# Optimization experiments

Hardware: AMD Instinct MI355X
Metric: run time of the kernel (lower is better)

The kernel has to match this reference:

```python
import jax, jax.numpy as jnp
import numpy as np

N, E, F, H = 50000, 800000, 128, 128


def setup_inputs() -> dict:
    key = jax.random.key(0)
    ks = jax.random.split(key, 12)
    senders = jax.random.randint(ks[2], (E,), 0, N)
    receivers = jnp.sort(jax.random.randint(ks[3], (E,), 0, N))
    # ensure segment ids span full node range so segment_sum covers all N rows
    receivers = receivers.at[0].set(0).at[-1].set(N - 1)
    s = 0.05
    return {
        "nodes": jax.random.normal(ks[0], (N, F), jnp.float32),
        "edges": jax.random.normal(ks[1], (E, F), jnp.float32),
        "senders": senders,
        "receivers": receivers,
        "Wm1": jax.random.normal(ks[4], (3 * F, H), jnp.float32) * s,
        "bm1": jnp.zeros((H,), jnp.float32),
        "Wm2": jax.random.normal(ks[5], (H, H), jnp.float32) * s,
        "bm2": jnp.zeros((H,), jnp.float32),
        "Wu1": jax.random.normal(ks[6], (F + H, H), jnp.float32) * s,
        "bu1": jnp.zeros((H,), jnp.float32),
        "Wu2": jax.random.normal(ks[7], (H, H), jnp.float32) * s,
        "bu2": jnp.zeros((H,), jnp.float32),
    }


def reference(nodes, edges, senders, receivers, Wm1, bm1, Wm2, bm2, Wu1, bu1, Wu2, bu2):
    n = nodes.shape[0]
    sender_feat = nodes[senders]      # [E, F] gather
    receiver_feat = nodes[receivers]  # [E, F] gather
    msg_in = jnp.concatenate([sender_feat, receiver_feat, edges], axis=-1)  # [E, 3F]
    messages = jax.nn.swish(msg_in @ Wm1 + bm1) @ Wm2 + bm2                 # [E, H]
    aggregated = jax.ops.segment_sum(messages, receivers, num_segments=n)   # [N, H]
    upd_in = jnp.concatenate([nodes, aggregated], axis=-1)                   # [N, F+H]
    return jax.nn.swish(upd_in @ Wu1 + bu1) @ Wu2 + bu2                      # [N, H]
```

## Files before the change

kernel.cpp:

```cpp
#include <hip/hip_runtime.h>
#include <hip/hip_bf16.h>


typedef __bf16 bf16_t;
typedef __bf16 bf16x8 __attribute__((ext_vector_type(8)));
typedef __bf16 bf16x4 __attribute__((ext_vector_type(4)));
typedef float f32x4 __attribute__((ext_vector_type(4)));

#define MFMA16(a, b, c) __builtin_amdgcn_mfma_f32_16x16x32_bf16((a), (b), (c), 0, 0, 0)

__device__ __forceinline__ bf16x8 cvt_bf16x8(f32x4 lo, f32x4 hi) {
  bf16x8 r;
  r[0] = (bf16_t)lo[0]; r[1] = (bf16_t)lo[1]; r[2] = (bf16_t)lo[2]; r[3] = (bf16_t)lo[3];
  r[4] = (bf16_t)hi[0]; r[5] = (bf16_t)hi[1]; r[6] = (bf16_t)hi[2]; r[7] = (bf16_t)hi[3];
  return r;
}

__device__ __forceinline__ float swishf(float x) { return x / (1.0f + __expf(-x)); }

__device__ __forceinline__ int pst_idx(int col, int e) {
  const int unit = (e >> 3) ^ (col & 7) ^ ((col >> 3) & 7);
  return col * 64 + unit * 8 + (e & 7);
}

__global__ void prep_kernel(const float* __restrict__ Wm1, const float* __restrict__ Wm2,
                            const float* __restrict__ Wu1, const float* __restrict__ Wu2,
                            const float* __restrict__ bm2,
                            bf16_t* __restrict__ WmabT, bf16_t* __restrict__ Wm1cT,
                            bf16_t* __restrict__ Wu1aT, bf16_t* __restrict__ WcT,
                            bf16_t* __restrict__ Wu2T, float* __restrict__ bvec) {
  const int t0 = blockIdx.x * blockDim.x + threadIdx.x;
  const int stride = gridDim.x * blockDim.x;
  for (int i = t0; i < 256 * 128; i += stride) {
    const int n = i >> 7, k = i & 127;
    const float v = (n < 128) ? Wm1[k * 128 + n] : Wm1[(128 + k) * 128 + (n - 128)];
    WmabT[i] = (bf16_t)v;
  }
  for (int i = t0; i < 128 * 128; i += stride) {
    const int n = i >> 7, k = i & 127;
    Wm1cT[i] = (bf16_t)Wm1[(256 + k) * 128 + n];
    Wu1aT[i] = (bf16_t)Wu1[k * 128 + n];
    Wu2T[i]  = (bf16_t)Wu2[k * 128 + n];
  }
  for (int i = t0; i < 128 * 128; i += stride) {
    const int r = i >> 7, c = i & 127;
    float acc = 0.f;
    for (int k = 0; k < 128; ++k) acc += Wm2[r * 128 + k] * Wu1[(128 + k) * 128 + c];
    WcT[c * 128 + r] = (bf16_t)acc;
  }
  if (t0 < 128) {
    float acc = 0.f;
    for (int k = 0; k < 128; ++k) acc += bm2[k] * Wu1[(128 + k) * 128 + t0];
    bvec[t0] = acc;
  }
}

__global__ __launch_bounds__(256) void node_pre_kernel(const float* __restrict__ nodes,
                                                       const bf16_t* __restrict__ WmabT,
                                                       const float* __restrict__ bm1,
                                                       bf16_t* __restrict__ P, const int nN) {
  const int tid = threadIdx.x;
  const int l = tid & 63, w = tid >> 6;
  const int wr = w >> 1, wc = w & 1;
  const int lr = l & 15, lk = l >> 4;
  const int half = blockIdx.y;
  const int r0 = blockIdx.x * 128 + wr * 64;
  const bf16_t* WT = WmabT + half * (128 * 128);

  f32x4 acc[4][4] = {};
#pragma unroll
  for (int ks = 0; ks < 4; ++ks) {
    bf16x8 a[4], b[4];
#pragma unroll
    for (int m = 0; m < 4; ++m) {
      int r = r0 + m * 16 + lr;
      if (r >= nN) r = nN - 1;
      const float* p = nodes + (long)r * 128 + ks * 32 + lk * 8;
      a[m] = cvt_bf16x8(*(const f32x4*)p, *(const f32x4*)(p + 4));
    }
#pragma unroll
    for (int n = 0; n < 4; ++n)
      b[n] = *(const bf16x8*)(WT + (wc * 64 + n * 16 + lr) * 128 + ks * 32 + lk * 8);
#pragma unroll
    for (int m = 0; m < 4; ++m)
#pragma unroll
      for (int n = 0; n < 4; ++n)
        acc[m][n] = MFMA16(a[m], b[n], acc[m][n]);
  }
#pragma unroll
  for (int m = 0; m < 4; ++m)
#pragma unroll
    for (int n = 0; n < 4; ++n)
#pragma unroll
      for (int j = 0; j < 4; ++j) {
        const int r = r0 + m * 16 + lk * 4 + j;
        const int c = wc * 64 + n * 16 + lr;
        const float bias = (half == 0) ? bm1[c] : 0.f;
        if (r < nN) P[(long)r * 256 + half * 128 + c] = (bf16_t)(acc[m][n][j] + bias);
      }
}

__global__ __launch_bounds__(256, 3) void edge_kernel(
    const float* __restrict__ edges, const int* __restrict__ senders,
    const int* __restrict__ receivers, const bf16_t* __restrict__ P,
    const bf16_t* __restrict__ Wm1cT, float* __restrict__ S, float* __restrict__ deg,
    const int ntiles) {
  __shared__ bf16_t Ws[128 * 128];
  __shared__ bf16_t PsT[128 * 64];
  __shared__ int runidL[64];
  __shared__ int runstartL[65];
  __shared__ int nrunsL;
  const int tid = threadIdx.x;
  const int lane = tid & 63, w = tid >> 6;
  const int lr = lane & 15, lk = lane >> 4;

#pragma unroll
  for (int i = 0; i < 8; ++i) {
    const int g = tid + i * 256;
    const int r = g >> 4, c = g & 15;
    const bf16x8 v = *(const bf16x8*)(Wm1cT + r * 128 + c * 8);
    *(bf16x8*)&Ws[r * 128 + ((c ^ (r & 15)) * 8)] = v;
  }

  const int nb = gridDim.x;
  const int cb = (blockIdx.x & 7) * (nb >> 3) + (blockIdx.x >> 3);
  const int q = ntiles / nb, r2 = ntiles % nb;
  const int tstart = cb * q + (cb < r2 ? cb : r2);
  const int tcnt = q + (cb < r2 ? 1 : 0);

  __syncthreads();

  for (int ti = 0; ti < tcnt; ++ti) {
    const long e0 = (long)(tstart + ti) * 64;
    const int eg = w * 16 + lr;

    const int sn = senders[e0 + eg];
    const int rn = receivers[e0 + eg];

    f32x4 Bf[4][2];
#pragma unroll
    for (int kc = 0; kc < 4; ++kc) {
      const f32x4* p = (const f32x4*)(edges + (e0 + eg) * 128 + kc * 32 + lk * 8);
      Bf[kc][0] = __builtin_nontemporal_load(p);
      Bf[kc][1] = __builtin_nontemporal_load(p + 1);
    }
    bf16x4 pa[8], pb[8];
#pragma unroll
    for (int m = 0; m < 8; ++m) {
      pa[m] = *(const bf16x4*)(P + (long)sn * 256 + m * 16 + lk * 4);
      pb[m] = *(const bf16x4*)(P + (long)rn * 256 + 128 + m * 16 + lk * 4);
    }

    if (w == 0) {
      const int myrcv = receivers[e0 + lane];
      const int prev = (lane == 0) ? -1 : receivers[e0 + lane - 1];
      const int head = (myrcv != prev) ? 1 : 0;
      const unsigned long long mask = __ballot(head);
      const int nruns = __popcll(mask);
      if (lane == 0) { nrunsL = nruns; runstartL[nruns] = 64; }
      if (head) {
        const int pre = __popcll(mask & ((1ull << lane) - 1));
        runidL[pre] = myrcv;
        runstartL[pre] = lane;
      }
    }

    f32x4 acc[8] = {};
#pragma unroll
    for (int kc = 0; kc < 4; ++kc) {
      const bf16x8 bb = cvt_bf16x8(Bf[kc][0], Bf[kc][1]);
#pragma unroll
      for (int m = 0; m < 8; ++m) {
        const bf16x8 aW = *(const bf16x8*)&Ws[(m * 16 + lr) * 128 + (((kc * 4 + lk) ^ lr) * 8)];
        acc[m] = MFMA16(aW, bb, acc[m]);
      }
    }

#pragma unroll
    for (int m = 0; m < 8; ++m)
#pragma unroll
      for (int j = 0; j < 4; ++j) {
        const int outcol = m * 16 + lk * 4 + j;
        const float x = acc[m][j] + (float)pa[m][j] + (float)pb[m][j];
        PsT[pst_idx(outcol, eg)] = (bf16_t)swishf(x);
      }
    __syncthreads();

    const int nruns = nrunsL;
    for (int nt = 0; nt * 16 < nruns; ++nt) {
      const int myrun = nt * 16 + lr;
      int lo = 64, hi = 64, myid = -1;
      if (myrun < nruns) {
        lo = runstartL[myrun];
        hi = runstartL[myrun + 1];
        myid = runidL[myrun];
      }
      f32x4 accS[2] = {};
#pragma unroll
      for (int kc = 0; kc < 2; ++kc) {
        bf16x8 bR;
#pragma unroll
        for (int j = 0; j < 8; ++j) {
          const int e = kc * 32 + lk * 8 + j;
          bR[j] = (e >= lo && e < hi) ? (bf16_t)1.0f : (bf16_t)0.0f;
        }
#pragma unroll
        for (int t = 0; t < 2; ++t) {
          const int col = (2 * w + t) * 16 + lr;
          const int unit = (kc * 4 + lk) ^ (col & 7) ^ ((col >> 3) & 7);
          const bf16x8 aH = *(const bf16x8*)&PsT[col * 64 + unit * 8];
          accS[t] = MFMA16(aH, bR, accS[t]);
        }
      }
      if (myrun < nruns) {
        const long base = (long)myid * 128;
        const bool boundary = (myrun == 0) || (myrun == nruns - 1);
#pragma unroll
        for (int t = 0; t < 2; ++t) {
          const int col0 = (2 * w + t) * 16 + lk * 4;
          if (boundary) {
#pragma unroll
            for (int j = 0; j < 4; ++j) unsafeAtomicAdd(&S[base + col0 + j], accS[t][j]);
          } else {
            *(f32x4*)(S + base + col0) = accS[t];
          }
        }
      }
    }

    if (tid < nruns) {
      const float len = (float)(runstartL[tid + 1] - runstartL[tid]);
      const int node = runidL[tid];
      if (tid == 0 || tid == nruns - 1) unsafeAtomicAdd(&deg[node], len);
      else deg[node] = len;
    }
    __syncthreads();
  }
}

__global__ __launch_bounds__(256) void node_out_kernel(
    const float* __restrict__ nodes, const float* __restrict__ S,
    const float* __restrict__ deg, const float* __restrict__ bvec,
    const float* __restrict__ bu1, const float* __restrict__ bu2,
    const bf16_t* __restrict__ Wu1aT, const bf16_t* __restrict__ WcT,
    const bf16_t* __restrict__ Wu2T, float* __restrict__ out, const int nN) {
  __shared__ bf16_t Hs[128 * 128];
  const int tid = threadIdx.x;
  const int l = tid & 63, w = tid >> 6;
  const int wr = w >> 1, wc = w & 1;
  const int lr = l & 15, lk = l >> 4;
  const int r0 = blockIdx.x * 128;

  f32x4 acc[4][4] = {};
#pragma unroll
  for (int src = 0; src < 2; ++src) {
    const float* X = src ? S : nodes;
    const bf16_t* WT = src ? WcT : Wu1aT;
#pragma unroll
    for (int ks = 0; ks < 4; ++ks) {
      bf16x8 a[4], b[4];
#pragma unroll
      for (int m = 0; m < 4; ++m) {
        int r = r0 + wr * 64 + m * 16 + lr;
        if (r >= nN) r = nN - 1;
        const float* p = X + (long)r * 128 + ks * 32 + lk * 8;
        a[m] = cvt_bf16x8(*(const f32x4*)p, *(const f32x4*)(p + 4));
      }
#pragma unroll
      for (int n = 0; n < 4; ++n)
        b[n] = *(const bf16x8*)(WT + (wc * 64 + n * 16 + lr) * 128 + ks * 32 + lk * 8);
#pragma unroll
      for (int m = 0; m < 4; ++m)
#pragma unroll
        for (int n = 0; n < 4; ++n)
          acc[m][n] = MFMA16(a[m], b[n], acc[m][n]);
    }
  }

#pragma unroll
  for (int m = 0; m < 4; ++m)
#pragma unroll
    for (int n = 0; n < 4; ++n)
#pragma unroll
      for (int j = 0; j < 4; ++j) {
        const int row = wr * 64 + m * 16 + lk * 4 + j;
        const int gr = r0 + row;
        const int col = wc * 64 + n * 16 + lr;
        const float dg = (gr < nN) ? deg[gr] : 0.f;
        const float x = acc[m][n][j] + bu1[col] + dg * bvec[col];
        Hs[row * 128 + (col ^ ((row & 7) << 3))] = (bf16_t)swishf(x);
      }
  __syncthreads();

  f32x4 acc2[4][4] = {};
#pragma unroll
  for (int ks = 0; ks < 4; ++ks) {
    bf16x8 a[4], b[4];
#pragma unroll
    for (int m = 0; m < 4; ++m) {
      const int r = wr * 64 + m * 16 + lr;
      a[m] = *(const bf16x8*)&Hs[r * 128 + ((ks * 32 + lk * 8) ^ ((r & 7) << 3))];
    }
#pragma unroll
    for (int n = 0; n < 4; ++n)
      b[n] = *(const bf16x8*)(Wu2T + (wc * 64 + n * 16 + lr) * 128 + ks * 32 + lk * 8);
#pragma unroll
    for (int m = 0; m < 4; ++m)
#pragma unroll
      for (int n = 0; n < 4; ++n)
        acc2[m][n] = MFMA16(a[m], b[n], acc2[m][n]);
  }

#pragma unroll
  for (int m = 0; m < 4; ++m)
#pragma unroll
    for (int n = 0; n < 4; ++n)
#pragma unroll
      for (int j = 0; j < 4; ++j) {
        const int row = r0 + wr * 64 + m * 16 + lk * 4 + j;
        const int col = wc * 64 + n * 16 + lr;
        if (row < nN) out[(long)row * 128 + col] = acc2[m][n][j] + bu2[col];
      }
}

extern "C" void kernel_launch(void* const* d_in, const int* in_sizes, int n_in,
                              void* d_out, int out_size, void* d_ws, size_t ws_size,
                              hipStream_t stream) {
  const float* nodes = (const float*)d_in[0];
  const float* edges = (const float*)d_in[1];
  const int* senders = (const int*)d_in[2];
  const int* receivers = (const int*)d_in[3];
  const float* Wm1 = (const float*)d_in[4];
  const float* bm1 = (const float*)d_in[5];
  const float* Wm2 = (const float*)d_in[6];
  const float* bm2 = (const float*)d_in[7];
  const float* Wu1 = (const float*)d_in[8];
  const float* bu1 = (const float*)d_in[9];
  const float* Wu2 = (const float*)d_in[10];
  const float* bu2 = (const float*)d_in[11];
  const int nN = in_sizes[0] / 128;
  const int nE = in_sizes[1] / 128;

  char* ws = (char*)d_ws;
  bf16_t* P = (bf16_t*)ws;
  float* S = (float*)(ws + (size_t)nN * 256 * 2);
  float* deg = S + (size_t)nN * 128;
  bf16_t* WmabT = (bf16_t*)(deg + nN);
  bf16_t* Wm1cT = WmabT + 256 * 128;
  bf16_t* Wu1aT = Wm1cT + 128 * 128;
  bf16_t* WcT = Wu1aT + 128 * 128;
  bf16_t* Wu2T = WcT + 128 * 128;
  float* bvec = (float*)(Wu2T + 128 * 128);

  hipMemsetAsync(S, 0, (size_t)nN * 129 * 4, stream);
  hipLaunchKernelGGL(prep_kernel, dim3(128), dim3(256), 0, stream,
                     Wm1, Wm2, Wu1, Wu2, bm2, WmabT, Wm1cT, Wu1aT, WcT, Wu2T, bvec);
  hipLaunchKernelGGL(node_pre_kernel, dim3((nN + 127) / 128, 2), dim3(256), 0, stream,
                     nodes, WmabT, bm1, P, nN);
  hipLaunchKernelGGL(edge_kernel, dim3(768), dim3(256), 0, stream,
                     edges, senders, receivers, P, Wm1cT, S, deg, nE / 64);
  hipLaunchKernelGGL(node_out_kernel, dim3((nN + 127) / 128), dim3(256), 0, stream,
                     nodes, S, deg, bvec, bu1, bu2, Wu1aT, WcT, Wu2T, (float*)d_out, nN);
}
```

Before: 287.1 us.

## Prefetch next edge tile's indices and features; replace memset with zero kernel

The edge kernel now loads the next tile's sender/receiver indices and edge feature rows into registers while the current tile is being processed, software-pipelining global memory latency across iterations. The hipMemsetAsync for the accumulator buffer is replaced with a custom vectorized zero kernel, possibly to avoid memset API overhead. The prefetch raises register pressure (an extra 8 f32x4 per lane), which could lower occupancy.

New measurement: 424.5 us. +47.8%, slower.

```diff
diff --git a/kernel.cpp b/kernel.cpp
--- a/kernel.cpp
+++ b/kernel.cpp
@@ -21,6 +21,12 @@
 __device__ __forceinline__ int pst_idx(int col, int e) {
   const int unit = (e >> 3) ^ (col & 7) ^ ((col >> 3) & 7);
   return col * 64 + unit * 8 + (e & 7);
+}
+
+__global__ __launch_bounds__(256) void zero_kernel(float* __restrict__ p, const long nvec) {
+  const long t0 = (long)blockIdx.x * blockDim.x + threadIdx.x;
+  const long stride = (long)gridDim.x * blockDim.x;
+  for (long i = t0; i < nvec; i += stride) *(f32x4*)(p + i * 4) = f32x4{0.f, 0.f, 0.f, 0.f};
 }
 
 __global__ void prep_kernel(const float* __restrict__ Wm1, const float* __restrict__ Wm2,
@@ -130,25 +136,42 @@
 
   __syncthreads();
 
-  for (int ti = 0; ti < tcnt; ++ti) {
-    const long e0 = (long)(tstart + ti) * 64;
-    const int eg = w * 16 + lr;
-
-    const int sn = senders[e0 + eg];
-    const int rn = receivers[e0 + eg];
-
-    f32x4 Bf[4][2];
+  const int eg = w * 16 + lr;
+
+  long e0 = (long)tstart * 64;
+  int sn = 0, rn = 0;
+  f32x4 Bf[4][2] = {};
+  if (tcnt > 0) {
+    sn = senders[e0 + eg];
+    rn = receivers[e0 + eg];
 #pragma unroll
     for (int kc = 0; kc < 4; ++kc) {
       const f32x4* p = (const f32x4*)(edges + (e0 + eg) * 128 + kc * 32 + lk * 8);
       Bf[kc][0] = __builtin_nontemporal_load(p);
       Bf[kc][1] = __builtin_nontemporal_load(p + 1);
     }
+  }
+
+  for (int ti = 0; ti < tcnt; ++ti) {
     bf16x4 pa[8], pb[8];
 #pragma unroll
     for (int m = 0; m < 8; ++m) {
       pa[m] = *(const bf16x4*)(P + (long)sn * 256 + m * 16 + lk * 4);
       pb[m] = *(const bf16x4*)(P + (long)rn * 256 + 128 + m * 16 + lk * 4);
+    }
+
+    const long e0n = e0 + 64;
+    int sn_n = 0, rn_n = 0;
+    f32x4 Bfn[4][2] = {};
+    if (ti + 1 < tcnt) {
+      sn_n = senders[e0n + eg];
+      rn_n = receivers[e0n + eg];
+#pragma unroll
+      for (int kc = 0; kc < 4; ++kc) {
+        const f32x4* p = (const f32x4*)(edges + (e0n + eg) * 128 + kc * 32 + lk * 8);
+        Bfn[kc][0] = __builtin_nontemporal_load(p);
+        Bfn[kc][1] = __builtin_nontemporal_load(p + 1);
+      }
     }
 
     if (w == 0) {
@@ -235,6 +258,13 @@
       else deg[node] = len;
     }
     __syncthreads();
+
+    e0 = e0n; sn = sn_n; rn = rn_n;
+#pragma unroll
+    for (int kc = 0; kc < 4; ++kc) {
+      Bf[kc][0] = Bfn[kc][0];
+      Bf[kc][1] = Bfn[kc][1];
+    }
   }
 }
 
@@ -352,7 +382,8 @@
   bf16_t* Wu2T = WcT + 128 * 128;
   float* bvec = (float*)(Wu2T + 128 * 128);
 
-  hipMemsetAsync(S, 0, (size_t)nN * 129 * 4, stream);
+  hipLaunchKernelGGL(zero_kernel, dim3(1024), dim3(256), 0, stream,
+                     S, (long)nN * 129 / 4);
   hipLaunchKernelGGL(prep_kernel, dim3(128), dim3(256), 0, stream,
                      Wm1, Wm2, Wu1, Wu2, bm2, WmabT, Wm1cT, Wu1aT, WcT, Wu2T, bvec);
   hipLaunchKernelGGL(node_pre_kernel, dim3((nN + 127) / 128, 2), dim3(256), 0, stream,
```

## Enlarge edge tiles to 128 edges per 512-thread block with coalesced P gathers

Applied to the files above, without the earlier changes.

The edge kernel now processes 128-edge tiles with 512-thread blocks. Sender/receiver projection rows are gathered cooperatively in 16-byte vectors and pre-summed into the shared transposed tile, and the swish step adds that stored sum to the MFMA result. Run detection spans two waves via shared ballot masks. The segment-sum MFMA loop now covers K=128 with one column tile per wave, and a custom zero kernel replaces the memset. The aim is to amortize weight loads and run boundaries over more edges and to coalesce the gathers, at the cost of doubled LDS (64 KB per block), an extra barrier and lower occupancy per CU.

After: 500.6 us. 74.4% more time.

```diff
diff --git a/kernel.cpp b/kernel.cpp
--- a/kernel.cpp
+++ b/kernel.cpp
@@ -4,7 +4,6 @@
 
 typedef __bf16 bf16_t;
 typedef __bf16 bf16x8 __attribute__((ext_vector_type(8)));
-typedef __bf16 bf16x4 __attribute__((ext_vector_type(4)));
 typedef float f32x4 __attribute__((ext_vector_type(4)));
 
 #define MFMA16(a, b, c) __builtin_amdgcn_mfma_f32_16x16x32_bf16((a), (b), (c), 0, 0, 0)
@@ -20,7 +19,13 @@
 
 __device__ __forceinline__ int pst_idx(int col, int e) {
   const int unit = (e >> 3) ^ (col & 7) ^ ((col >> 3) & 7);
-  return col * 64 + unit * 8 + (e & 7);
+  return col * 128 + unit * 8 + (e & 7);
+}
+
+__global__ __launch_bounds__(256) void zero_kernel(float* __restrict__ p, const long nvec) {
+  const long t0 = (long)blockIdx.x * blockDim.x + threadIdx.x;
+  const long stride = (long)gridDim.x * blockDim.x;
+  for (long i = t0; i < nvec; i += stride) *(f32x4*)(p + i * 4) = f32x4{0.f, 0.f, 0.f, 0.f};
 }
 
 __global__ void prep_kernel(const float* __restrict__ Wm1, const float* __restrict__ Wm2,
@@ -100,23 +105,24 @@
       }
 }
 
-__global__ __launch_bounds__(256, 3) void edge_kernel(
+__global__ __launch_bounds__(512, 4) void edge_kernel(
     const float* __restrict__ edges, const int* __restrict__ senders,
     const int* __restrict__ receivers, const bf16_t* __restrict__ P,
     const bf16_t* __restrict__ Wm1cT, float* __restrict__ S, float* __restrict__ deg,
     const int ntiles) {
   __shared__ bf16_t Ws[128 * 128];
-  __shared__ bf16_t PsT[128 * 64];
-  __shared__ int runidL[64];
-  __shared__ int runstartL[65];
+  __shared__ bf16_t PsT[128 * 128];
+  __shared__ int runidL[128];
+  __shared__ int runstartL[129];
+  __shared__ unsigned long long maskL[2];
   __shared__ int nrunsL;
   const int tid = threadIdx.x;
   const int lane = tid & 63, w = tid >> 6;
   const int lr = lane & 15, lk = lane >> 4;
 
 #pragma unroll
-  for (int i = 0; i < 8; ++i) {
-    const int g = tid + i * 256;
+  for (int i = 0; i < 4; ++i) {
+    const int g = tid + i * 512;
     const int r = g >> 4, c = g & 15;
     const bf16x8 v = *(const bf16x8*)(Wm1cT + r * 128 + c * 8);
     *(bf16x8*)&Ws[r * 128 + ((c ^ (r & 15)) * 8)] = v;
@@ -130,12 +136,10 @@
 
   __syncthreads();
 
+  const int eg = w * 16 + lr;
+
   for (int ti = 0; ti < tcnt; ++ti) {
-    const long e0 = (long)(tstart + ti) * 64;
-    const int eg = w * 16 + lr;
-
-    const int sn = senders[e0 + eg];
-    const int rn = receivers[e0 + eg];
+    const long e0 = (long)(tstart + ti) * 128;
 
     f32x4 Bf[4][2];
 #pragma unroll
@@ -144,24 +148,28 @@
       Bf[kc][0] = __builtin_nontemporal_load(p);
       Bf[kc][1] = __builtin_nontemporal_load(p + 1);
     }
-    bf16x4 pa[8], pb[8];
-#pragma unroll
-    for (int m = 0; m < 8; ++m) {
-      pa[m] = *(const bf16x4*)(P + (long)sn * 256 + m * 16 + lk * 4);
-      pb[m] = *(const bf16x4*)(P + (long)rn * 256 + 128 + m * 16 + lk * 4);
-    }
-
-    if (w == 0) {
-      const int myrcv = receivers[e0 + lane];
-      const int prev = (lane == 0) ? -1 : receivers[e0 + lane - 1];
-      const int head = (myrcv != prev) ? 1 : 0;
+
+    int head = 0, myrcv = 0;
+    if (tid < 128) {
+      myrcv = receivers[e0 + tid];
+      const int prev = (tid == 0) ? -1 : receivers[e0 + tid - 1];
+      head = (myrcv != prev) ? 1 : 0;
       const unsigned long long mask = __ballot(head);
-      const int nruns = __popcll(mask);
-      if (lane == 0) { nrunsL = nruns; runstartL[nruns] = 64; }
-      if (head) {
-        const int pre = __popcll(mask & ((1ull << lane) - 1));
-        runidL[pre] = myrcv;
-        runstartL[pre] = lane;
+      if ((tid & 63) == 0) maskL[tid >> 6] = mask;
+    }
+
+#pragma unroll
+    for (int i = 0; i < 4; ++i) {
+      const int c = tid + i * 512;
+      const int row = c >> 4, k = c & 15;
+      const int sn = senders[e0 + row];
+      const int rn = receivers[e0 + row];
+      const bf16x8 pa = *(const bf16x8*)(P + (long)sn * 256 + k * 8);
+      const bf16x8 pb = *(const bf16x8*)(P + (long)rn * 256 + 128 + k * 8);
+#pragma unroll
+      for (int j = 0; j < 8; ++j) {
+        const float v = (float)pa[j] + (float)pb[j];
+        PsT[pst_idx(k * 8 + j, row)] = (bf16_t)v;
       }
     }
 
@@ -175,55 +183,63 @@
         acc[m] = MFMA16(aW, bb, acc[m]);
       }
     }
+    __syncthreads();
+
+    if (tid < 128) {
+      const unsigned long long m0 = maskL[0], m1 = maskL[1];
+      const int nruns = __popcll(m0) + __popcll(m1);
+      if (tid == 0) { nrunsL = nruns; runstartL[nruns] = 128; }
+      if (head) {
+        const unsigned long long mymask = (tid < 64) ? m0 : m1;
+        int pre = __popcll(mymask & ((1ull << (tid & 63)) - 1));
+        if (tid >= 64) pre += __popcll(m0);
+        runidL[pre] = myrcv;
+        runstartL[pre] = tid;
+      }
+    }
 
 #pragma unroll
     for (int m = 0; m < 8; ++m)
 #pragma unroll
       for (int j = 0; j < 4; ++j) {
         const int outcol = m * 16 + lk * 4 + j;
-        const float x = acc[m][j] + (float)pa[m][j] + (float)pb[m][j];
-        PsT[pst_idx(outcol, eg)] = (bf16_t)swishf(x);
+        const int idx = pst_idx(outcol, eg);
+        const float x = acc[m][j] + (float)PsT[idx];
+        PsT[idx] = (bf16_t)swishf(x);
       }
     __syncthreads();
 
     const int nruns = nrunsL;
     for (int nt = 0; nt * 16 < nruns; ++nt) {
       const int myrun = nt * 16 + lr;
-      int lo = 64, hi = 64, myid = -1;
+      int lo = 128, hi = 128, myid = -1;
       if (myrun < nruns) {
         lo = runstartL[myrun];
         hi = runstartL[myrun + 1];
         myid = runidL[myrun];
       }
-      f32x4 accS[2] = {};
-#pragma unroll
-      for (int kc = 0; kc < 2; ++kc) {
+      f32x4 accS = {};
+#pragma unroll
+      for (int kc = 0; kc < 4; ++kc) {
         bf16x8 bR;
 #pragma unroll
         for (int j = 0; j < 8; ++j) {
           const int e = kc * 32 + lk * 8 + j;
           bR[j] = (e >= lo && e < hi) ? (bf16_t)1.0f : (bf16_t)0.0f;
         }
-#pragma unroll
-        for (int t = 0; t < 2; ++t) {
-          const int col = (2 * w + t) * 16 + lr;
-          const int unit = (kc * 4 + lk) ^ (col & 7) ^ ((col >> 3) & 7);
-          const bf16x8 aH = *(const bf16x8*)&PsT[col * 64 + unit * 8];
-          accS[t] = MFMA16(aH, bR, accS[t]);
-        }
+        const int col = w * 16 + lr;
+        const int unit = (kc * 4 + lk) ^ (col & 7) ^ ((col >> 3) & 7);
+        const bf16x8 aH = *(const bf16x8*)&PsT[col * 128 + unit * 8];
+        accS = MFMA16(aH, bR, accS);
       }
       if (myrun < nruns) {
         const long base = (long)myid * 128;
-        const bool boundary = (myrun == 0) || (myrun == nruns - 1);
-#pragma unroll
-        for (int t = 0; t < 2; ++t) {
-          const int col0 = (2 * w + t) * 16 + lk * 4;
-          if (boundary) {
-#pragma unroll
-            for (int j = 0; j < 4; ++j) unsafeAtomicAdd(&S[base + col0 + j], accS[t][j]);
-          } else {
-            *(f32x4*)(S + base + col0) = accS[t];
-          }
+        const int col0 = w * 16 + lk * 4;
+        if (myrun == 0 || myrun == nruns - 1) {
+#pragma unroll
+          for (int j = 0; j < 4; ++j) unsafeAtomicAdd(&S[base + col0 + j], accS[j]);
+        } else {
+          *(f32x4*)(S + base + col0) = accS;
         }
       }
     }
@@ -352,13 +368,14 @@
   bf16_t* Wu2T = WcT + 128 * 128;
   float* bvec = (float*)(Wu2T + 128 * 128);
 
-  hipMemsetAsync(S, 0, (size_t)nN * 129 * 4, stream);
+  hipLaunchKernelGGL(zero_kernel, dim3(1024), dim3(256), 0, stream,
+                     S, (long)nN * 129 / 4);
   hipLaunchKernelGGL(prep_kernel, dim3(128), dim3(256), 0, stream,
                      Wm1, Wm2, Wu1, Wu2, bm2, WmabT, Wm1cT, Wu1aT, WcT, Wu2T, bvec);
   hipLaunchKernelGGL(node_pre_kernel, dim3((nN + 127) / 128, 2), dim3(256), 0, stream,
                      nodes, WmabT, bm1, P, nN);
-  hipLaunchKernelGGL(edge_kernel, dim3(768), dim3(256), 0, stream,
-                     edges, senders, receivers, P, Wm1cT, S, deg, nE / 64);
+  hipLaunchKernelGGL(edge_kernel, dim3(512), dim3(512), 0, stream,
+                     edges, senders, receivers, P, Wm1cT, S, deg, nE / 128);
   hipLaunchKernelGGL(node_out_kernel, dim3((nN + 127) / 128), dim3(256), 0, stream,
                      nodes, S, deg, bvec, bu1, bu2, Wu1aT, WcT, Wu2T, (float*)d_out, nN);
 }
```

## Prefetch next edge tile in edge kernel and fold memset into prep kernel

Applied to the files above, without the earlier changes.

The edge kernel now loads the next tile's edge features and sender/receiver indices right after the swish write barrier, so those global loads overlap with the segment-sum phase of the current tile instead of stalling at the top of each iteration. Separately, zeroing of the aggregation buffer moves from a hipMemsetAsync into the prep kernel, whose grid grows to 1024 blocks, removing one launch. The prefetch keeps more live registers across the loop and may lower occupancy. The vectorized zeroing relies on nN*129 being divisible by 4, which holds for N=50000.

New measurement: 342.7 us. 19.4% more time.

```diff
diff --git a/kernel.cpp b/kernel.cpp
--- a/kernel.cpp
+++ b/kernel.cpp
@@ -23,14 +23,18 @@
   return col * 64 + unit * 8 + (e & 7);
 }
 
-__global__ void prep_kernel(const float* __restrict__ Wm1, const float* __restrict__ Wm2,
-                            const float* __restrict__ Wu1, const float* __restrict__ Wu2,
-                            const float* __restrict__ bm2,
-                            bf16_t* __restrict__ WmabT, bf16_t* __restrict__ Wm1cT,
-                            bf16_t* __restrict__ Wu1aT, bf16_t* __restrict__ WcT,
-                            bf16_t* __restrict__ Wu2T, float* __restrict__ bvec) {
+__global__ __launch_bounds__(256) void prep_kernel(
+    const float* __restrict__ Wm1, const float* __restrict__ Wm2,
+    const float* __restrict__ Wu1, const float* __restrict__ Wu2,
+    const float* __restrict__ bm2,
+    bf16_t* __restrict__ WmabT, bf16_t* __restrict__ Wm1cT,
+    bf16_t* __restrict__ Wu1aT, bf16_t* __restrict__ WcT,
+    bf16_t* __restrict__ Wu2T, float* __restrict__ bvec,
+    float* __restrict__ Sz, const long nvec) {
   const int t0 = blockIdx.x * blockDim.x + threadIdx.x;
   const int stride = gridDim.x * blockDim.x;
+  for (long i = t0; i < nvec; i += stride)
+    *(f32x4*)(Sz + i * 4) = f32x4{0.f, 0.f, 0.f, 0.f};
   for (int i = t0; i < 256 * 128; i += stride) {
     const int n = i >> 7, k = i & 127;
     const float v = (n < 128) ? Wm1[k * 128 + n] : Wm1[(128 + k) * 128 + (n - 128)];
@@ -130,20 +134,25 @@
 
   __syncthreads();
 
+  const int eg = w * 16 + lr;
+
+  f32x4 Bf[4][2];
+  int sn = 0, rn = 0;
+  if (tcnt > 0) {
+    const long e0p = (long)tstart * 64;
+#pragma unroll
+    for (int kc = 0; kc < 4; ++kc) {
+      const f32x4* p = (const f32x4*)(edges + (e0p + eg) * 128 + kc * 32 + lk * 8);
+      Bf[kc][0] = __builtin_nontemporal_load(p);
+      Bf[kc][1] = __builtin_nontemporal_load(p + 1);
+    }
+    sn = senders[e0p + eg];
+    rn = receivers[e0p + eg];
+  }
+
   for (int ti = 0; ti < tcnt; ++ti) {
     const long e0 = (long)(tstart + ti) * 64;
-    const int eg = w * 16 + lr;
-
-    const int sn = senders[e0 + eg];
-    const int rn = receivers[e0 + eg];
-
-    f32x4 Bf[4][2];
-#pragma unroll
-    for (int kc = 0; kc < 4; ++kc) {
-      const f32x4* p = (const f32x4*)(edges + (e0 + eg) * 128 + kc * 32 + lk * 8);
-      Bf[kc][0] = __builtin_nontemporal_load(p);
-      Bf[kc][1] = __builtin_nontemporal_load(p + 1);
-    }
+
     bf16x4 pa[8], pb[8];
 #pragma unroll
     for (int m = 0; m < 8; ++m) {
@@ -185,6 +194,18 @@
         PsT[pst_idx(outcol, eg)] = (bf16_t)swishf(x);
       }
     __syncthreads();
+
+    if (ti + 1 < tcnt) {
+      const long e1 = e0 + 64;
+#pragma unroll
+      for (int kc = 0; kc < 4; ++kc) {
+        const f32x4* p = (const f32x4*)(edges + (e1 + eg) * 128 + kc * 32 + lk * 8);
+        Bf[kc][0] = __builtin_nontemporal_load(p);
+        Bf[kc][1] = __builtin_nontemporal_load(p + 1);
+      }
+      sn = senders[e1 + eg];
+      rn = receivers[e1 + eg];
+    }
 
     const int nruns = nrunsL;
     for (int nt = 0; nt * 16 < nruns; ++nt) {
@@ -352,9 +373,9 @@
   bf16_t* Wu2T = WcT + 128 * 128;
   float* bvec = (float*)(Wu2T + 128 * 128);
 
-  hipMemsetAsync(S, 0, (size_t)nN * 129 * 4, stream);
-  hipLaunchKernelGGL(prep_kernel, dim3(128), dim3(256), 0, stream,
-                     Wm1, Wm2, Wu1, Wu2, bm2, WmabT, Wm1cT, Wu1aT, WcT, Wu2T, bvec);
+  hipLaunchKernelGGL(prep_kernel, dim3(1024), dim3(256), 0, stream,
+                     Wm1, Wm2, Wu1, Wu2, bm2, WmabT, Wm1cT, Wu1aT, WcT, Wu2T, bvec,
+                     S, (long)nN * 129 / 4);
   hipLaunchKernelGGL(node_pre_kernel, dim3((nN + 127) / 128, 2), dim3(256), 0, stream,
                      nodes, WmabT, bm1, P, nN);
   hipLaunchKernelGGL(edge_kernel, dim3(768), dim3(256), 0, stream,
```
